# Optimization experiments

Hardware: AMD Instinct MI355X
Metric: run time of the kernel (lower is better)

Reference implementation:

```python
import jax, jax.numpy as jnp
import numpy as np

Q = 0.8  # quantile used for frequency thresholding


def dct_mat(N, dtype=jnp.float32):
    """Orthonormal DCT-II matrix M, so dct(v) = M @ v and idct(u) = M.T @ u."""
    n = jnp.arange(N)
    k = n[:, None]
    M = jnp.cos(jnp.pi * (2 * n[None, :] + 1) * k / (2 * N))
    s = jnp.full((N,), jnp.sqrt(2.0 / N)).at[0].set(jnp.sqrt(1.0 / N))
    return (s[:, None] * M).astype(dtype)


def setup_inputs() -> dict:
    key = jax.random.key(0)
    B, T, C = 64, 576, 1024  # batch, tokens (24x24 patches), ViT-L width
    x = jax.random.normal(key, (B, T, C), dtype=jnp.float32)
    return {"x": x}


def reference(x):
    # Faithful translation of DCTLAVISBlip.dc_transform(x, use_reconstucted_freq=True).
    # Torch works in (T,B,C)/(C,B,T) layouts; math is DCT/IDCT along the token axis,
    # which we express directly on the [B, T, C] layout (outputs already permuted to
    # batch-first, matching the torch returns).
    B, T, C = x.shape
    M = dct_mat(T, x.dtype)
    # DCT-II (ortho) over tokens: freq axis k.  [B, T, C]
    x_dct = jnp.einsum('btc,kt->bkc', x, M)
    # |mean over batch then over channels| per frequency -> (T,)
    x_dct_mean = jnp.abs(x_dct.mean(axis=0).mean(axis=-1))
    threshold = jnp.abs(jnp.quantile(x_dct_mean, Q))
    # Data-dependent truncation index (host-side, as in the torch .item() call).
    idxs = np.where(np.asarray(x_dct_mean > threshold))[0]
    last_index = int(idxs[-1]) if idxs.size > 0 else -1
    x_dct_trunc = x_dct[:, :last_index, :]  # [B, L, C]; last_index=-1 drops 1 row, as in torch
    L = x_dct_trunc.shape[1]
    # IDCT (DCT-III, ortho) on the truncated length-L sequence.
    Mi = dct_mat(L, x.dtype)
    state = jnp.einsum('blc,lk->bkc', x_dct_trunc, Mi).astype(jnp.float16)  # [B, L, C]
    return state, x_dct_trunc
```

## Files before the change

kernel.cpp:

```cpp
#include <hip/hip_runtime.h>
#include <hip/hip_bf16.h>

typedef _Float16 f16;
typedef _Float16 f16x4 __attribute__((ext_vector_type(4)));
typedef _Float16 f16x8 __attribute__((ext_vector_type(8)));
typedef float f32x4 __attribute__((ext_vector_type(4)));

#define B_    64
#define T_    576
#define C_    1024
#define KDIM  576
#define MPAD  640

__device__ __forceinline__ void gload_lds16(const void* g, void* l) {
  __builtin_amdgcn_global_load_lds(
      (__attribute__((address_space(1))) void*)(void*)g,
      (__attribute__((address_space(3))) void*)l, 16, 0, 0);
}

__global__ void gen_mats(f16* __restrict__ Mh,
                         f16* __restrict__ MTh, f16* __restrict__ MTl,
                         f16* __restrict__ MiTh, f16* __restrict__ MiTl, int L) {
  int idx = blockIdx.x * 256 + threadIdx.x;
  if (idx >= MPAD * KDIM) return;
  int row = idx / KDIM;
  int col = idx - row * KDIM;
  const float pif = 3.14159265358979323846f;
  float v = 0.0f;
  if (blockIdx.y == 0) {
    if (row < T_) {
      float a = pif * (float)(2 * col + 1);
      a = a * (float)row;
      a = a / 1152.0f;
      float s = (row == 0) ? sqrtf((float)(1.0 / 576.0)) : sqrtf((float)(2.0 / 576.0));
      v = s * cosf(a);
    }
    Mh[idx] = (f16)v;
  } else if (blockIdx.y == 1) {
    if (row < T_) {
      float a = pif * (float)(2 * row + 1);
      a = a * (float)col;
      a = a / 1152.0f;
      float s = (col == 0) ? sqrtf((float)(1.0 / 576.0)) : sqrtf((float)(2.0 / 576.0));
      v = s * cosf(a);
    }
    f16 h = (f16)v;
    MTh[idx] = h;
    MTl[idx] = (f16)(v - (float)h);
  } else {
    if (row < L && col < L) {
      float a = pif * (float)(2 * row + 1);
      a = a * (float)col;
      a = a / (float)(2 * L);
      float s = (col == 0) ? sqrtf((float)(1.0 / (double)L))
                           : sqrtf((float)(2.0 / (double)L));
      v = s * cosf(a);
    }
    f16 h = (f16)v;
    MiTh[idx] = h;
    MiTl[idx] = (f16)(v - (float)h);
  }
}

__global__ void gemm_G(const f16* __restrict__ gAh, const f16* __restrict__ gAl,
                       const f16* __restrict__ gBh, const f16* __restrict__ gBl,
                       f16* __restrict__ G) {
  __shared__ __align__(16) f16 sAh[128 * 32];
  __shared__ __align__(16) f16 sAl[128 * 32];
  __shared__ __align__(16) f16 sBh[128 * 32];
  __shared__ __align__(16) f16 sBl[128 * 32];
  const int tid = threadIdx.x, lane = tid & 63, wid = tid >> 6;
  const int m0 = blockIdx.y * 128, n0 = blockIdx.x * 128;
  const int wr = wid >> 1, wc = wid & 1;
  const int l15 = lane & 15, lg = lane >> 4;

  f32x4 acc[4][4];
#pragma unroll
  for (int i = 0; i < 4; ++i)
#pragma unroll
    for (int j = 0; j < 4; ++j) acc[i][j] = (f32x4){0.f, 0.f, 0.f, 0.f};

  for (int kt = 0; kt < KDIM; kt += 32) {
    __syncthreads();
#pragma unroll
    for (int it = 0; it < 2; ++it) {
      const int o = it * 4096 + tid * 16;
      const int r = o >> 6, cb = o & 63;
      gload_lds16((const char*)gAh + ((size_t)(m0 + r) * KDIM + kt) * 2 + cb, (char*)sAh + o);
      gload_lds16((const char*)gAl + ((size_t)(m0 + r) * KDIM + kt) * 2 + cb, (char*)sAl + o);
      gload_lds16((const char*)gBh + ((size_t)(n0 + r) * KDIM + kt) * 2 + cb, (char*)sBh + o);
      gload_lds16((const char*)gBl + ((size_t)(n0 + r) * KDIM + kt) * 2 + cb, (char*)sBl + o);
    }
    __syncthreads();

    f16x8 ah[4], al[4], bh[4], bl[4];
#pragma unroll
    for (int i = 0; i < 4; ++i) {
      const int ra = (wr * 64 + i * 16 + l15) * 32 + lg * 8;
      ah[i] = *(const f16x8*)&sAh[ra];
      al[i] = *(const f16x8*)&sAl[ra];
      const int rb = (wc * 64 + i * 16 + l15) * 32 + lg * 8;
      bh[i] = *(const f16x8*)&sBh[rb];
      bl[i] = *(const f16x8*)&sBl[rb];
    }
#pragma unroll
    for (int i = 0; i < 4; ++i)
#pragma unroll
      for (int j = 0; j < 4; ++j) {
        acc[i][j] = __builtin_amdgcn_mfma_f32_16x16x32_f16(ah[i], bh[j], acc[i][j], 0, 0, 0);
        acc[i][j] = __builtin_amdgcn_mfma_f32_16x16x32_f16(ah[i], bl[j], acc[i][j], 0, 0, 0);
        acc[i][j] = __builtin_amdgcn_mfma_f32_16x16x32_f16(al[i], bh[j], acc[i][j], 0, 0, 0);
      }
  }

#pragma unroll
  for (int i = 0; i < 4; ++i) {
    const int t4 = m0 + wr * 64 + i * 16 + lg * 4;
#pragma unroll
    for (int j = 0; j < 4; ++j) {
      const int k = n0 + wc * 64 + j * 16 + l15;
      if (t4 < T_) {
        f32x4 v = acc[i][j];
        f16x4 hv;
#pragma unroll
        for (int r = 0; r < 4; ++r) hv[r] = (f16)v[r];
        *(f16x4*)&G[(size_t)k * KDIM + t4] = hv;
      }
    }
  }
}

__global__ void transpose_f16(const float* __restrict__ x, f16* __restrict__ XT) {
  __shared__ float tile[64][65];
  const int b = blockIdx.z;
  const int t0 = blockIdx.y * 64, c0 = blockIdx.x * 64;
  const int i = threadIdx.x;
  const float* xp = x + ((size_t)b * T_ + t0) * C_ + c0;
  const int lrow = i >> 4, lcq = (i & 15) * 4;
#pragma unroll
  for (int p = 0; p < 4; ++p) {
    int r = p * 16 + lrow;
    float4 v = *(const float4*)&xp[(size_t)r * C_ + lcq];
    tile[r][lcq + 0] = v.x; tile[r][lcq + 1] = v.y;
    tile[r][lcq + 2] = v.z; tile[r][lcq + 3] = v.w;
  }
  __syncthreads();
  const int tg = (i & 7) * 8, cl = i >> 3;
#pragma unroll
  for (int h = 0; h < 2; ++h) {
    int c = cl + h * 32;
    f16x8 o;
#pragma unroll
    for (int u = 0; u < 8; ++u) o[u] = (f16)tile[tg + u][c];
    *(f16x8*)&XT[((size_t)b * C_ + c0 + c) * T_ + t0 + tg] = o;
  }
}

__global__ void gemm_main(const f16* __restrict__ gM, const f16* __restrict__ gG,
                          const f16* __restrict__ gXT,
                          float* __restrict__ out_trunc, float* __restrict__ out_state,
                          int L) {
  __shared__ __align__(16) f16 sA[128 * 32];
  __shared__ __align__(16) f16 sB[128 * 32];

  const int tid = threadIdx.x, lane = tid & 63, wid = tid >> 6;
  const int z = blockIdx.z, b = z >> 1, stage = z & 1;
  const int m0 = blockIdx.y * 128, n0 = blockIdx.x * 128;
  const int wr = wid >> 1, wc = wid & 1;
  const int l15 = lane & 15, lg = lane >> 4;

  const f16* gA = stage ? gG : gM;
  const f16* bb = gXT + (size_t)b * C_ * KDIM;

  f32x4 acc[4][4];
#pragma unroll
  for (int i = 0; i < 4; ++i)
#pragma unroll
    for (int j = 0; j < 4; ++j) acc[i][j] = (f32x4){0.f, 0.f, 0.f, 0.f};

  for (int kt = 0; kt < KDIM; kt += 32) {
    __syncthreads();
#pragma unroll
    for (int it = 0; it < 2; ++it) {
      const int o = it * 4096 + tid * 16;
      const int r = o >> 6, cb = o & 63;
      gload_lds16((const char*)gA + ((size_t)(m0 + r) * KDIM + kt) * 2 + cb,
                  (char*)sA + o);
      gload_lds16((const char*)bb + ((size_t)(n0 + r) * KDIM + kt) * 2 + cb,
                  (char*)sB + o);
    }
    __syncthreads();

    f16x8 af[4], bf[4];
#pragma unroll
    for (int i = 0; i < 4; ++i) {
      af[i] = *(const f16x8*)&sA[(wr * 64 + i * 16 + l15) * 32 + lg * 8];
      bf[i] = *(const f16x8*)&sB[(wc * 64 + i * 16 + l15) * 32 + lg * 8];
    }
#pragma unroll
    for (int i = 0; i < 4; ++i)
#pragma unroll
      for (int j = 0; j < 4; ++j)
        acc[i][j] = __builtin_amdgcn_mfma_f32_16x16x32_f16(af[i], bf[j], acc[i][j], 0, 0, 0);
  }

  float* outp = stage ? out_state : out_trunc;
#pragma unroll
  for (int i = 0; i < 4; ++i) {
    const int k0 = m0 + wr * 64 + i * 16 + lg * 4;
#pragma unroll
    for (int j = 0; j < 4; ++j) {
      const int c = n0 + wc * 64 + j * 16 + l15;
      f32x4 v = acc[i][j];
#pragma unroll
      for (int r = 0; r < 4; ++r) {
        const int k = k0 + r;
        if (k < L) {
          float val = v[r];
          if (stage) val = (float)(f16)val;
          outp[((size_t)b * L + k) * C_ + c] = val;
        }
      }
    }
  }
}

extern "C" void kernel_launch(void* const* d_in, const int* in_sizes, int n_in,
                              void* d_out, int out_size, void* d_ws, size_t ws_size,
                              hipStream_t stream) {
  (void)in_sizes; (void)n_in;
  const float* x = (const float*)d_in[0];

  const int L = out_size / (2 * B_ * C_);
  const int mtiles = (L + 127) / 128;
  float* out_state = (float*)d_out;
  float* out_trunc = out_state + (size_t)B_ * L * C_;

  char* w = (char*)d_ws;
  const size_t SZ_XT = (size_t)B_ * C_ * KDIM * sizeof(f16);
  const size_t SZ_M  = (size_t)MPAD * KDIM * sizeof(f16);
  if (ws_size < SZ_XT + 6 * SZ_M) return;

  f16* XT   = (f16*)(w);
  f16* Mh   = (f16*)(w + SZ_XT);
  f16* Gh   = (f16*)(w + SZ_XT + 1 * SZ_M);
  f16* MTh  = (f16*)(w + SZ_XT + 2 * SZ_M);
  f16* MTl  = (f16*)(w + SZ_XT + 3 * SZ_M);
  f16* MiTh = (f16*)(w + SZ_XT + 4 * SZ_M);
  f16* MiTl = (f16*)(w + SZ_XT + 5 * SZ_M);

  gen_mats<<<dim3((MPAD * KDIM + 255) / 256, 3), 256, 0, stream>>>(
      Mh, MTh, MTl, MiTh, MiTl, L);
  gemm_G<<<dim3(MPAD / 128, MPAD / 128), 256, 0, stream>>>(
      MTh, MTl, MiTh, MiTl, Gh);
  transpose_f16<<<dim3(C_ / 64, T_ / 64, B_), 256, 0, stream>>>(x, XT);
  gemm_main<<<dim3(C_ / 128, mtiles, 2 * B_), 256, 0, stream>>>(
      Mh, Gh, XT, out_trunc, out_state, L);
}
```

Before: 530.7 us.

## Stack DCT and composed IDCT matrices into one 256x256 double-buffered GEMM

The DCT matrix rows (first L) and the precomputed G = Mi^T·M rows are stacked into one A operand, so a single GEMM per batch produces both outputs instead of two separate stage launches. The main GEMM moves to 256x256 tiles with 512 threads, BK=64, double-buffered LDS with async global-to-LDS loads, XOR-swizzled LDS addressing and raised MFMA priority. This increases reuse of the XT operand, avoids padding waste from two separate mtile ranges, and overlaps loads with compute. The cost is larger LDS and register use per block, which limits occupancy, and a dependence on G being written at row offset L in the stacked buffer.

```diff
diff --git a/kernel.cpp b/kernel.cpp
--- a/kernel.cpp
+++ b/kernel.cpp
@@ -11,6 +11,9 @@
 #define C_    1024
 #define KDIM  576
 #define MPAD  640
+#define AROWS 1280
+#define BK    64
+#define NT    9
 
 __device__ __forceinline__ void gload_lds16(const void* g, void* l) {
   __builtin_amdgcn_global_load_lds(
@@ -18,25 +21,28 @@
       (__attribute__((address_space(3))) void*)l, 16, 0, 0);
 }
 
-__global__ void gen_mats(f16* __restrict__ Mh,
+__global__ void gen_mats(f16* __restrict__ Astk,
                          f16* __restrict__ MTh, f16* __restrict__ MTl,
                          f16* __restrict__ MiTh, f16* __restrict__ MiTl, int L) {
   int idx = blockIdx.x * 256 + threadIdx.x;
-  if (idx >= MPAD * KDIM) return;
-  int row = idx / KDIM;
-  int col = idx - row * KDIM;
   const float pif = 3.14159265358979323846f;
   float v = 0.0f;
   if (blockIdx.y == 0) {
-    if (row < T_) {
+    if (idx >= AROWS * KDIM) return;
+    int row = idx / KDIM;
+    int col = idx - row * KDIM;
+    if (row < L) {
       float a = pif * (float)(2 * col + 1);
       a = a * (float)row;
       a = a / 1152.0f;
       float s = (row == 0) ? sqrtf((float)(1.0 / 576.0)) : sqrtf((float)(2.0 / 576.0));
       v = s * cosf(a);
     }
-    Mh[idx] = (f16)v;
+    Astk[idx] = (f16)v;
   } else if (blockIdx.y == 1) {
+    if (idx >= MPAD * KDIM) return;
+    int row = idx / KDIM;
+    int col = idx - row * KDIM;
     if (row < T_) {
       float a = pif * (float)(2 * row + 1);
       a = a * (float)col;
@@ -48,6 +54,9 @@
     MTh[idx] = h;
     MTl[idx] = (f16)(v - (float)h);
   } else {
+    if (idx >= MPAD * KDIM) return;
+    int row = idx / KDIM;
+    int col = idx - row * KDIM;
     if (row < L && col < L) {
       float a = pif * (float)(2 * row + 1);
       a = a * (float)col;
@@ -64,7 +73,7 @@
 
 __global__ void gemm_G(const f16* __restrict__ gAh, const f16* __restrict__ gAl,
                        const f16* __restrict__ gBh, const f16* __restrict__ gBl,
-                       f16* __restrict__ G) {
+                       f16* __restrict__ Astk, int L) {
   __shared__ __align__(16) f16 sAh[128 * 32];
   __shared__ __align__(16) f16 sAl[128 * 32];
   __shared__ __align__(16) f16 sBh[128 * 32];
@@ -124,7 +133,7 @@
         f16x4 hv;
 #pragma unroll
         for (int r = 0; r < 4; ++r) hv[r] = (f16)v[r];
-        *(f16x4*)&G[(size_t)k * KDIM + t4] = hv;
+        *(f16x4*)&Astk[(size_t)(L + k) * KDIM + t4] = hv;
       }
     }
   }
@@ -156,69 +165,116 @@
   }
 }
 
-__global__ void gemm_main(const f16* __restrict__ gM, const f16* __restrict__ gG,
-                          const f16* __restrict__ gXT,
-                          float* __restrict__ out_trunc, float* __restrict__ out_state,
-                          int L) {
-  __shared__ __align__(16) f16 sA[128 * 32];
-  __shared__ __align__(16) f16 sB[128 * 32];
-
-  const int tid = threadIdx.x, lane = tid & 63, wid = tid >> 6;
-  const int z = blockIdx.z, b = z >> 1, stage = z & 1;
-  const int m0 = blockIdx.y * 128, n0 = blockIdx.x * 128;
-  const int wr = wid >> 1, wc = wid & 1;
+__global__ __launch_bounds__(512, 2)
+void gemm256(const f16* __restrict__ gA, const f16* __restrict__ gXT,
+             float* __restrict__ out_trunc, float* __restrict__ out_state,
+             int L) {
+  __shared__ __align__(16) f16 ldsA[2][256 * BK];
+  __shared__ __align__(16) f16 ldsB[2][256 * BK];
+
+  const int tid = threadIdx.x;
+  const int lane = tid & 63, wid = tid >> 6;
+  const int wm = wid >> 2, wn = wid & 3;
+  const int b = blockIdx.z;
+  const int m0 = blockIdx.y * 256, n0 = blockIdx.x * 256;
   const int l15 = lane & 15, lg = lane >> 4;
-
-  const f16* gA = stage ? gG : gM;
-  const f16* bb = gXT + (size_t)b * C_ * KDIM;
-
-  f32x4 acc[4][4];
-#pragma unroll
-  for (int i = 0; i < 4; ++i)
+  const f16* gB = gXT + (size_t)b * C_ * KDIM;
+
+  int srow[4], scol[4];
+#pragma unroll
+  for (int i = 0; i < 4; ++i) {
+    const int o = i * 8192 + tid * 16;
+    srow[i] = o >> 7;
+    scol[i] = (o & 127) ^ ((srow[i] & 7) << 4);
+  }
+
+#define STAGE(tile_, buf_)                                                        \
+  {                                                                               \
+    const int ktb_ = (tile_) * (BK * 2);                                          \
+    _Pragma("unroll") for (int i = 0; i < 4; ++i) {                               \
+      gload_lds16((const char*)gA + (size_t)(m0 + srow[i]) * (KDIM * 2) + ktb_ +  \
+                      scol[i],                                                    \
+                  (char*)&ldsA[buf_][0] + i * 8192 + tid * 16);                   \
+    }                                                                             \
+    _Pragma("unroll") for (int i = 0; i < 4; ++i) {                               \
+      gload_lds16((const char*)gB + (size_t)(n0 + srow[i]) * (KDIM * 2) + ktb_ +  \
+                      scol[i],                                                    \
+                  (char*)&ldsB[buf_][0] + i * 8192 + tid * 16);                   \
+    }                                                                             \
+  }
+
+  f32x4 acc[8][4];
+#pragma unroll
+  for (int i = 0; i < 8; ++i)
 #pragma unroll
     for (int j = 0; j < 4; ++j) acc[i][j] = (f32x4){0.f, 0.f, 0.f, 0.f};
 
-  for (int kt = 0; kt < KDIM; kt += 32) {
-    __syncthreads();
-#pragma unroll
-    for (int it = 0; it < 2; ++it) {
-      const int o = it * 4096 + tid * 16;
-      const int r = o >> 6, cb = o & 63;
-      gload_lds16((const char*)gA + ((size_t)(m0 + r) * KDIM + kt) * 2 + cb,
-                  (char*)sA + o);
-      gload_lds16((const char*)bb + ((size_t)(n0 + r) * KDIM + kt) * 2 + cb,
-                  (char*)sB + o);
-    }
-    __syncthreads();
-
-    f16x8 af[4], bf[4];
-#pragma unroll
-    for (int i = 0; i < 4; ++i) {
-      af[i] = *(const f16x8*)&sA[(wr * 64 + i * 16 + l15) * 32 + lg * 8];
-      bf[i] = *(const f16x8*)&sB[(wc * 64 + i * 16 + l15) * 32 + lg * 8];
-    }
-#pragma unroll
-    for (int i = 0; i < 4; ++i)
-#pragma unroll
-      for (int j = 0; j < 4; ++j)
-        acc[i][j] = __builtin_amdgcn_mfma_f32_16x16x32_f16(af[i], bf[j], acc[i][j], 0, 0, 0);
-  }
-
-  float* outp = stage ? out_state : out_trunc;
-#pragma unroll
-  for (int i = 0; i < 4; ++i) {
-    const int k0 = m0 + wr * 64 + i * 16 + lg * 4;
-#pragma unroll
-    for (int j = 0; j < 4; ++j) {
-      const int c = n0 + wc * 64 + j * 16 + l15;
-      f32x4 v = acc[i][j];
+  const int xorv = (l15 & 7) << 4;
+  const int eac0 = ((0 * 64 + lg * 16) ^ xorv) >> 1;
+  const int eac1 = ((1 * 64 + lg * 16) ^ xorv) >> 1;
+  const int arb = wm * 128 + l15;
+  const int brb = wn * 64 + l15;
+
+  STAGE(0, 0);
+  STAGE(1, 1);
+
+  for (int t = 0; t < NT; ++t) {
+    if (t == NT - 1) {
+      asm volatile("s_waitcnt vmcnt(0)" ::: "memory");
+    } else {
+      asm volatile("s_waitcnt vmcnt(8)" ::: "memory");
+    }
+    asm volatile("s_barrier" ::: "memory");
+    const f16* sA = &ldsA[t & 1][0];
+    const f16* sB = &ldsB[t & 1][0];
+
+    f16x8 bf[4][2];
+#pragma unroll
+    for (int nf = 0; nf < 4; ++nf) {
+      bf[nf][0] = *(const f16x8*)&sB[(brb + nf * 16) * BK + eac0];
+      bf[nf][1] = *(const f16x8*)&sB[(brb + nf * 16) * BK + eac1];
+    }
+#pragma unroll
+    for (int ph = 0; ph < 4; ++ph) {
+      f16x8 af[2][2];
+#pragma unroll
+      for (int mf = 0; mf < 2; ++mf) {
+        const int ar = (arb + ph * 32 + mf * 16) * BK;
+        af[mf][0] = *(const f16x8*)&sA[ar + eac0];
+        af[mf][1] = *(const f16x8*)&sA[ar + eac1];
+      }
+      __builtin_amdgcn_s_setprio(1);
+#pragma unroll
+      for (int ks = 0; ks < 2; ++ks)
+#pragma unroll
+        for (int mf = 0; mf < 2; ++mf)
+#pragma unroll
+          for (int nf = 0; nf < 4; ++nf)
+            acc[ph * 2 + mf][nf] = __builtin_amdgcn_mfma_f32_16x16x32_f16(
+                af[mf][ks], bf[nf][ks], acc[ph * 2 + mf][nf], 0, 0, 0);
+      __builtin_amdgcn_s_setprio(0);
+    }
+
+    asm volatile("s_waitcnt lgkmcnt(0)" ::: "memory");
+    asm volatile("s_barrier" ::: "memory");
+    if (t + 2 < NT) STAGE(t + 2, t & 1);
+  }
+
+  const int L2 = 2 * L;
+#pragma unroll
+  for (int mi = 0; mi < 8; ++mi) {
+    const int kk0 = m0 + wm * 128 + mi * 16 + lg * 4;
+#pragma unroll
+    for (int nf = 0; nf < 4; ++nf) {
+      const int c = n0 + wn * 64 + nf * 16 + l15;
+      f32x4 v = acc[mi][nf];
 #pragma unroll
       for (int r = 0; r < 4; ++r) {
-        const int k = k0 + r;
-        if (k < L) {
-          float val = v[r];
-          if (stage) val = (float)(f16)val;
-          outp[((size_t)b * L + k) * C_ + c] = val;
+        const int kk = kk0 + r;
+        if (kk < L) {
+          out_trunc[((size_t)b * L + kk) * C_ + c] = v[r];
+        } else if (kk < L2) {
+          out_state[((size_t)b * L + (kk - L)) * C_ + c] = (float)(f16)v[r];
         }
       }
     }
@@ -232,28 +288,28 @@
   const float* x = (const float*)d_in[0];
 
   const int L = out_size / (2 * B_ * C_);
-  const int mtiles = (L + 127) / 128;
+  const int mtiles = (2 * L + 255) / 256;
   float* out_state = (float*)d_out;
   float* out_trunc = out_state + (size_t)B_ * L * C_;
 
   char* w = (char*)d_ws;
   const size_t SZ_XT = (size_t)B_ * C_ * KDIM * sizeof(f16);
+  const size_t SZ_A  = (size_t)AROWS * KDIM * sizeof(f16);
   const size_t SZ_M  = (size_t)MPAD * KDIM * sizeof(f16);
-  if (ws_size < SZ_XT + 6 * SZ_M) return;
+  if (ws_size < SZ_XT + SZ_A + 4 * SZ_M) return;
 
   f16* XT   = (f16*)(w);
-  f16* Mh   = (f16*)(w + SZ_XT);
-  f16* Gh   = (f16*)(w + SZ_XT + 1 * SZ_M);
-  f16* MTh  = (f16*)(w + SZ_XT + 2 * SZ_M);
-  f16* MTl  = (f16*)(w + SZ_XT + 3 * SZ_M);
-  f16* MiTh = (f16*)(w + SZ_XT + 4 * SZ_M);
-  f16* MiTl = (f16*)(w + SZ_XT + 5 * SZ_M);
-
-  gen_mats<<<dim3((MPAD * KDIM + 255) / 256, 3), 256, 0, stream>>>(
-      Mh, MTh, MTl, MiTh, MiTl, L);
+  f16* Astk = (f16*)(w + SZ_XT);
+  f16* MTh  = (f16*)(w + SZ_XT + SZ_A);
+  f16* MTl  = (f16*)(w + SZ_XT + SZ_A + 1 * SZ_M);
+  f16* MiTh = (f16*)(w + SZ_XT + SZ_A + 2 * SZ_M);
+  f16* MiTl = (f16*)(w + SZ_XT + SZ_A + 3 * SZ_M);
+
+  gen_mats<<<dim3((AROWS * KDIM + 255) / 256, 3), 256, 0, stream>>>(
+      Astk, MTh, MTl, MiTh, MiTl, L);
   gemm_G<<<dim3(MPAD / 128, MPAD / 128), 256, 0, stream>>>(
-      MTh, MTl, MiTh, MiTl, Gh);
+      MTh, MTl, MiTh, MiTl, Astk, L);
   transpose_f16<<<dim3(C_ / 64, T_ / 64, B_), 256, 0, stream>>>(x, XT);
-  gemm_main<<<dim3(C_ / 128, mtiles, 2 * B_), 256, 0, stream>>>(
-      Mh, Gh, XT, out_trunc, out_state, L);
-}
+  gemm256<<<dim3(C_ / 256, mtiles, B_), 512, 0, stream>>>(
+      Astk, XT, out_trunc, out_state, L);
+}
```

Result: slower. 544.8 us (+2.6%).

## Fuse transpose with matrix generation and double K-tile depth in main GEMM

Applied to the files above, without the earlier changes.

Merges the fp32-to-fp16 transpose of x and the DCT matrix generation into one launch, removing a kernel launch and letting the two independent jobs overlap. The main GEMM now stages 64-wide K tiles in LDS instead of 32, which halves the barriers per output tile at the cost of doubling LDS per block (possible occupancy loss). The M-tile count is hardcoded to 5 instead of computed from L, which is only safe while L stays at or below 640.

```diff
diff --git a/kernel.cpp b/kernel.cpp
--- a/kernel.cpp
+++ b/kernel.cpp
@@ -11,6 +11,7 @@
 #define C_    1024
 #define KDIM  576
 #define MPAD  640
+#define TRBLK (16 * 9 * 64)
 
 __device__ __forceinline__ void gload_lds16(const void* g, void* l) {
   __builtin_amdgcn_global_load_lds(
@@ -18,47 +19,77 @@
       (__attribute__((address_space(3))) void*)l, 16, 0, 0);
 }
 
-__global__ void gen_mats(f16* __restrict__ Mh,
-                         f16* __restrict__ MTh, f16* __restrict__ MTl,
-                         f16* __restrict__ MiTh, f16* __restrict__ MiTl, int L) {
-  int idx = blockIdx.x * 256 + threadIdx.x;
-  if (idx >= MPAD * KDIM) return;
-  int row = idx / KDIM;
-  int col = idx - row * KDIM;
-  const float pif = 3.14159265358979323846f;
-  float v = 0.0f;
-  if (blockIdx.y == 0) {
-    if (row < T_) {
-      float a = pif * (float)(2 * col + 1);
-      a = a * (float)row;
-      a = a / 1152.0f;
-      float s = (row == 0) ? sqrtf((float)(1.0 / 576.0)) : sqrtf((float)(2.0 / 576.0));
-      v = s * cosf(a);
-    }
-    Mh[idx] = (f16)v;
-  } else if (blockIdx.y == 1) {
-    if (row < T_) {
-      float a = pif * (float)(2 * row + 1);
-      a = a * (float)col;
-      a = a / 1152.0f;
-      float s = (col == 0) ? sqrtf((float)(1.0 / 576.0)) : sqrtf((float)(2.0 / 576.0));
-      v = s * cosf(a);
-    }
-    f16 h = (f16)v;
-    MTh[idx] = h;
-    MTl[idx] = (f16)(v - (float)h);
+__global__ void prep(const float* __restrict__ x, f16* __restrict__ XT,
+                     f16* __restrict__ Mh,
+                     f16* __restrict__ MTh, f16* __restrict__ MTl,
+                     f16* __restrict__ MiTh, f16* __restrict__ MiTl, int L) {
+  __shared__ float tile[64][65];
+  const int tb = blockIdx.x;
+  if (tb < TRBLK) {
+    const int b = tb / 144, rem = tb % 144;
+    const int c0 = (rem & 15) * 64, t0 = (rem >> 4) * 64;
+    const int i = threadIdx.x;
+    const float* xp = x + ((size_t)b * T_ + t0) * C_ + c0;
+    const int lrow = i >> 4, lcq = (i & 15) * 4;
+#pragma unroll
+    for (int p = 0; p < 4; ++p) {
+      int r = p * 16 + lrow;
+      float4 v = *(const float4*)&xp[(size_t)r * C_ + lcq];
+      tile[r][lcq + 0] = v.x; tile[r][lcq + 1] = v.y;
+      tile[r][lcq + 2] = v.z; tile[r][lcq + 3] = v.w;
+    }
+    __syncthreads();
+    const int tg = (i & 7) * 8, cl = i >> 3;
+#pragma unroll
+    for (int h = 0; h < 2; ++h) {
+      int c = cl + h * 32;
+      f16x8 o;
+#pragma unroll
+      for (int u = 0; u < 8; ++u) o[u] = (f16)tile[tg + u][c];
+      *(f16x8*)&XT[((size_t)b * C_ + c0 + c) * T_ + t0 + tg] = o;
+    }
   } else {
-    if (row < L && col < L) {
-      float a = pif * (float)(2 * row + 1);
-      a = a * (float)col;
-      a = a / (float)(2 * L);
-      float s = (col == 0) ? sqrtf((float)(1.0 / (double)L))
-                           : sqrtf((float)(2.0 / (double)L));
-      v = s * cosf(a);
-    }
-    f16 h = (f16)v;
-    MiTh[idx] = h;
-    MiTl[idx] = (f16)(v - (float)h);
+    const int g = tb - TRBLK;
+    const int y = g / 1440;
+    const int idx = (g - y * 1440) * 256 + threadIdx.x;
+    if (idx >= MPAD * KDIM) return;
+    const int row = idx / KDIM;
+    const int col = idx - row * KDIM;
+    const float pif = 3.14159265358979323846f;
+    float v = 0.0f;
+    if (y == 0) {
+      if (row < T_) {
+        float a = pif * (float)(2 * col + 1);
+        a = a * (float)row;
+        a = a / 1152.0f;
+        float s = (row == 0) ? sqrtf((float)(1.0 / 576.0)) : sqrtf((float)(2.0 / 576.0));
+        v = s * cosf(a);
+      }
+      Mh[idx] = (f16)v;
+    } else if (y == 1) {
+      if (row < T_) {
+        float a = pif * (float)(2 * row + 1);
+        a = a * (float)col;
+        a = a / 1152.0f;
+        float s = (col == 0) ? sqrtf((float)(1.0 / 576.0)) : sqrtf((float)(2.0 / 576.0));
+        v = s * cosf(a);
+      }
+      f16 h = (f16)v;
+      MTh[idx] = h;
+      MTl[idx] = (f16)(v - (float)h);
+    } else {
+      if (row < L && col < L) {
+        float a = pif * (float)(2 * row + 1);
+        a = a * (float)col;
+        a = a / (float)(2 * L);
+        float s = (col == 0) ? sqrtf((float)(1.0 / (double)L))
+                             : sqrtf((float)(2.0 / (double)L));
+        v = s * cosf(a);
+      }
+      f16 h = (f16)v;
+      MiTh[idx] = h;
+      MiTl[idx] = (f16)(v - (float)h);
+    }
   }
 }
 
@@ -130,38 +161,12 @@
   }
 }
 
-__global__ void transpose_f16(const float* __restrict__ x, f16* __restrict__ XT) {
-  __shared__ float tile[64][65];
-  const int b = blockIdx.z;
-  const int t0 = blockIdx.y * 64, c0 = blockIdx.x * 64;
-  const int i = threadIdx.x;
-  const float* xp = x + ((size_t)b * T_ + t0) * C_ + c0;
-  const int lrow = i >> 4, lcq = (i & 15) * 4;
-#pragma unroll
-  for (int p = 0; p < 4; ++p) {
-    int r = p * 16 + lrow;
-    float4 v = *(const float4*)&xp[(size_t)r * C_ + lcq];
-    tile[r][lcq + 0] = v.x; tile[r][lcq + 1] = v.y;
-    tile[r][lcq + 2] = v.z; tile[r][lcq + 3] = v.w;
-  }
-  __syncthreads();
-  const int tg = (i & 7) * 8, cl = i >> 3;
-#pragma unroll
-  for (int h = 0; h < 2; ++h) {
-    int c = cl + h * 32;
-    f16x8 o;
-#pragma unroll
-    for (int u = 0; u < 8; ++u) o[u] = (f16)tile[tg + u][c];
-    *(f16x8*)&XT[((size_t)b * C_ + c0 + c) * T_ + t0 + tg] = o;
-  }
-}
-
 __global__ void gemm_main(const f16* __restrict__ gM, const f16* __restrict__ gG,
                           const f16* __restrict__ gXT,
                           float* __restrict__ out_trunc, float* __restrict__ out_state,
                           int L) {
-  __shared__ __align__(16) f16 sA[128 * 32];
-  __shared__ __align__(16) f16 sB[128 * 32];
+  __shared__ __align__(16) f16 sA[128 * 64];
+  __shared__ __align__(16) f16 sB[128 * 64];
 
   const int tid = threadIdx.x, lane = tid & 63, wid = tid >> 6;
   const int z = blockIdx.z, b = z >> 1, stage = z & 1;
@@ -178,30 +183,33 @@
 #pragma unroll
     for (int j = 0; j < 4; ++j) acc[i][j] = (f32x4){0.f, 0.f, 0.f, 0.f};
 
-  for (int kt = 0; kt < KDIM; kt += 32) {
-    __syncthreads();
-#pragma unroll
-    for (int it = 0; it < 2; ++it) {
+  for (int kt = 0; kt < KDIM; kt += 64) {
+    __syncthreads();
+#pragma unroll
+    for (int it = 0; it < 4; ++it) {
       const int o = it * 4096 + tid * 16;
-      const int r = o >> 6, cb = o & 63;
-      gload_lds16((const char*)gA + ((size_t)(m0 + r) * KDIM + kt) * 2 + cb,
+      const int r = o >> 7, cb = o & 127;
+      gload_lds16((const char*)gA + (size_t)(m0 + r) * (KDIM * 2) + kt * 2 + cb,
                   (char*)sA + o);
-      gload_lds16((const char*)bb + ((size_t)(n0 + r) * KDIM + kt) * 2 + cb,
+      gload_lds16((const char*)bb + (size_t)(n0 + r) * (KDIM * 2) + kt * 2 + cb,
                   (char*)sB + o);
     }
     __syncthreads();
 
-    f16x8 af[4], bf[4];
-#pragma unroll
-    for (int i = 0; i < 4; ++i) {
-      af[i] = *(const f16x8*)&sA[(wr * 64 + i * 16 + l15) * 32 + lg * 8];
-      bf[i] = *(const f16x8*)&sB[(wc * 64 + i * 16 + l15) * 32 + lg * 8];
-    }
-#pragma unroll
-    for (int i = 0; i < 4; ++i)
-#pragma unroll
-      for (int j = 0; j < 4; ++j)
-        acc[i][j] = __builtin_amdgcn_mfma_f32_16x16x32_f16(af[i], bf[j], acc[i][j], 0, 0, 0);
+#pragma unroll
+    for (int ks = 0; ks < 2; ++ks) {
+      f16x8 af[4], bf[4];
+#pragma unroll
+      for (int i = 0; i < 4; ++i) {
+        af[i] = *(const f16x8*)&sA[(wr * 64 + i * 16 + l15) * 64 + ks * 32 + lg * 8];
+        bf[i] = *(const f16x8*)&sB[(wc * 64 + i * 16 + l15) * 64 + ks * 32 + lg * 8];
+      }
+#pragma unroll
+      for (int i = 0; i < 4; ++i)
+#pragma unroll
+        for (int j = 0; j < 4; ++j)
+          acc[i][j] = __builtin_amdgcn_mfma_f32_16x16x32_f16(af[i], bf[j], acc[i][j], 0, 0, 0);
+    }
   }
 
   float* outp = stage ? out_state : out_trunc;
@@ -232,7 +240,6 @@
   const float* x = (const float*)d_in[0];
 
   const int L = out_size / (2 * B_ * C_);
-  const int mtiles = (L + 127) / 128;
   float* out_state = (float*)d_out;
   float* out_trunc = out_state + (size_t)B_ * L * C_;
 
@@ -249,11 +256,10 @@
   f16* MiTh = (f16*)(w + SZ_XT + 4 * SZ_M);
   f16* MiTl = (f16*)(w + SZ_XT + 5 * SZ_M);
 
-  gen_mats<<<dim3((MPAD * KDIM + 255) / 256, 3), 256, 0, stream>>>(
-      Mh, MTh, MTl, MiTh, MiTl, L);
+  prep<<<TRBLK + 3 * 1440, 256, 0, stream>>>(
+      x, XT, Mh, MTh, MTl, MiTh, MiTl, L);
   gemm_G<<<dim3(MPAD / 128, MPAD / 128), 256, 0, stream>>>(
       MTh, MTl, MiTh, MiTl, Gh);
-  transpose_f16<<<dim3(C_ / 64, T_ / 64, B_), 256, 0, stream>>>(x, XT);
-  gemm_main<<<dim3(C_ / 128, mtiles, 2 * B_), 256, 0, stream>>>(
+  gemm_main<<<dim3(C_ / 128, 5, 2 * B_), 256, 0, stream>>>(
       Mh, Gh, XT, out_trunc, out_state, L);
 }
```

New measurement: 523.8 us. Within noise of the previous version (-1.3%).
